# Kernel tuning notes

Hardware: AMD Instinct MI355X
Metric: run time of the kernel (lower is better)

## Reference

```python
import jax, jax.numpy as jnp
import numpy as np

B, C, T = 1024, 64, 512
D, H = 32, 4
DK = D // H  # 8
EPS = 1e-5


def setup_inputs() -> dict:
    key = jax.random.key(0)
    ks = jax.random.split(key, 10)
    s_in = 1.0 / np.sqrt(T)
    s_d = 1.0 / np.sqrt(D)
    return {
        "x": jax.random.normal(ks[0], (B, C, T), dtype=jnp.float32),
        "W_in": jax.random.uniform(ks[1], (T, D), jnp.float32, -s_in, s_in),
        "b_in": jax.random.uniform(ks[2], (D,), jnp.float32, -s_in, s_in),
        "W_q": jax.random.uniform(ks[3], (D, D), jnp.float32, -s_d, s_d),
        "W_k": jax.random.uniform(ks[4], (D, D), jnp.float32, -s_d, s_d),
        "W_v": jax.random.uniform(ks[5], (D, D), jnp.float32, -s_d, s_d),
        "W_out": jax.random.uniform(ks[6], (D, T), jnp.float32, -s_d, s_d),
        "b_out": jax.random.uniform(ks[7], (T,), jnp.float32, -s_d, s_d),
        "gamma": jnp.ones((T,), jnp.float32),
        "beta": jnp.zeros((T,), jnp.float32),
    }


def reference(x, W_in, b_in, W_q, W_k, W_v, W_out, b_out, gamma, beta):
    # x: (B, C, T) -> project time dim to d_model
    h = jnp.einsum("bct,td->bcd", x, W_in) + b_in  # (B,C,D)
    q = (h @ W_q).reshape(B, C, H, DK)
    k = (h @ W_k).reshape(B, C, H, DK)
    v = (h @ W_v).reshape(B, C, H, DK)
    # attention over channel axis; scores (B,H,C,C)
    scores = jnp.einsum("bchd,bkhd->bhck", q, k) / np.sqrt(DK).astype(np.float32)
    attn = jax.nn.softmax(scores, axis=-1)  # dropout is identity at inference
    out = jnp.einsum("bhck,bkhd->bchd", attn, v).reshape(B, C, D)
    out = out @ W_out + b_out  # (B,C,T); proj_out dropout is identity
    y = out + x  # residual
    mu = jnp.mean(y, axis=-1, keepdims=True)
    var = jnp.var(y, axis=-1, keepdims=True)
    return (y - mu) * jax.lax.rsqrt(var + EPS) * gamma + beta
```

## Files before the change

kernel.cpp:

```cpp
#include <hip/hip_runtime.h>

typedef __attribute__((ext_vector_type(8))) short bf16x8;
typedef __attribute__((ext_vector_type(4))) float f32x4;

#define NB 1024
#define NC 64
#define NT 512
#define ND 32
#define NH 4

__device__ __forceinline__ unsigned short f2bf(float f) {
  unsigned u = __float_as_uint(f);
  u += 0x7FFFu + ((u >> 16) & 1u);
  return (unsigned short)(u >> 16);
}

__global__ void prep_weights(const float* __restrict__ Win, const float* __restrict__ Wq,
                             const float* __restrict__ Wk, const float* __restrict__ Wv,
                             const float* __restrict__ Wout, unsigned short* __restrict__ ws) {
  int idx = blockIdx.x * 256 + threadIdx.x;
  if (idx >= 35840) return;
  float v;
  if (idx < 16384) {
    int j = idx & 7, lane = (idx >> 3) & 63, nt = (idx >> 9) & 1, ks = idx >> 10;
    int t = 32 * ks + 8 * (lane >> 4) + j;
    int d = 16 * nt + (lane & 15);
    v = Win[t * ND + d];
  } else if (idx < 32768) {
    int p = idx - 16384;
    int j = p & 7, lane = (p >> 3) & 63, nt = (p >> 9) & 31;
    int k = 8 * (lane >> 4) + j;
    int n = 16 * nt + (lane & 15);
    v = Wout[k * NT + n];
  } else {
    int p = idx - 32768;
    const float* W = (p < 1024) ? Wq : ((p < 2048) ? Wk : Wv);
    int q = p & 1023;
    int j = q & 7, lane = (q >> 3) & 63, nt = (q >> 9) & 1;
    int t = 8 * (lane >> 4) + j;
    int d = 16 * nt + (lane & 15);
    v = W[t * ND + d];
  }
  ws[idx] = f2bf(v);
}

__global__ __launch_bounds__(256, 2)
void mha_main(const float* __restrict__ x, const float* __restrict__ b_in,
              const float* __restrict__ b_out, const float* __restrict__ gamma,
              const float* __restrict__ beta, const unsigned short* __restrict__ wsb,
              float* __restrict__ out) {
  __shared__ __align__(16) unsigned short lds_h[4][64][8];
  __shared__ __align__(16) unsigned short lds_o[4][64][8];
  __shared__ __align__(16) float lds_q[64][36];
  __shared__ __align__(16) float lds_k[64][36];
  __shared__ __align__(16) float lds_v[64][36];
  __shared__ float lds_red0[4][64];
  __shared__ float lds_red1[4][64];
  __shared__ float lds_mu[64];
  __shared__ float lds_rs[64];

  const int tid = threadIdx.x;
  const int w  = tid >> 6;
  const int l  = tid & 63;
  const int g  = l >> 4;
  const int lo = l & 15;
  const int b  = blockIdx.x;
  const float* __restrict__ xb = x + (size_t)b * (NC * NT);

  const int srow = 16 * w + lo;
  const float* __restrict__ xr = xb + srow * NT + 8 * g;
  const bf16x8* __restrict__ wsWin = (const bf16x8*)wsb;

  f32x4 acc1[2];
  acc1[0] = (f32x4){0.f, 0.f, 0.f, 0.f};
  acc1[1] = (f32x4){0.f, 0.f, 0.f, 0.f};
  f32x4 ra = *(const f32x4*)(xr);
  f32x4 rb = *(const f32x4*)(xr + 4);
  bf16x8 bp0 = wsWin[l];
  bf16x8 bp1 = wsWin[64 + l];

#pragma unroll
  for (int ks = 0; ks < 16; ++ks) {
    bf16x8 af;
    af[0] = (short)f2bf(ra[0]); af[1] = (short)f2bf(ra[1]);
    af[2] = (short)f2bf(ra[2]); af[3] = (short)f2bf(ra[3]);
    af[4] = (short)f2bf(rb[0]); af[5] = (short)f2bf(rb[1]);
    af[6] = (short)f2bf(rb[2]); af[7] = (short)f2bf(rb[3]);
    int nk = (ks < 15) ? (ks + 1) : 15;
    f32x4 ra2 = *(const f32x4*)(xr + 32 * nk);
    f32x4 rb2 = *(const f32x4*)(xr + 32 * nk + 4);
    bf16x8 bn0 = wsWin[(2 * nk) * 64 + l];
    bf16x8 bn1 = wsWin[(2 * nk + 1) * 64 + l];
    acc1[0] = __builtin_amdgcn_mfma_f32_16x16x32_bf16(af, bp0, acc1[0], 0, 0, 0);
    acc1[1] = __builtin_amdgcn_mfma_f32_16x16x32_bf16(af, bp1, acc1[1], 0, 0, 0);
    ra = ra2; rb = rb2; bp0 = bn0; bp1 = bn1;
  }

  float binv0 = b_in[lo];
  float binv1 = b_in[16 + lo];
#pragma unroll
  for (int nt = 0; nt < 2; ++nt) {
#pragma unroll
    for (int r = 0; r < 4; ++r) {
      float hv = acc1[nt][r] + (nt ? binv1 : binv0);
      int cc = 2 * nt + (lo >> 3);
      int slotlane = (4 * g + r) | (cc << 4);
      lds_h[w][slotlane][lo & 7] = f2bf(hv);
    }
  }
  __syncthreads();

  const bf16x8* __restrict__ wsWq = (const bf16x8*)(wsb + 32768);
  const bf16x8* __restrict__ wsWk = (const bf16x8*)(wsb + 33792);
  const bf16x8* __restrict__ wsWv = (const bf16x8*)(wsb + 34816);
  bf16x8 ah = *(const bf16x8*)&lds_h[w][l][0];
  f32x4 zero4 = (f32x4){0.f, 0.f, 0.f, 0.f};
  f32x4 qacc[2], kacc[2], vacc[2];
#pragma unroll
  for (int nt = 0; nt < 2; ++nt) {
    qacc[nt] = __builtin_amdgcn_mfma_f32_16x16x32_bf16(ah, wsWq[nt * 64 + l], zero4, 0, 0, 0);
    kacc[nt] = __builtin_amdgcn_mfma_f32_16x16x32_bf16(ah, wsWk[nt * 64 + l], zero4, 0, 0, 0);
    vacc[nt] = __builtin_amdgcn_mfma_f32_16x16x32_bf16(ah, wsWv[nt * 64 + l], zero4, 0, 0, 0);
  }
#pragma unroll
  for (int nt = 0; nt < 2; ++nt) {
#pragma unroll
    for (int r = 0; r < 4; ++r) {
      int row = 16 * w + 4 * g + r;
      int col = 16 * nt + lo;
      lds_q[row][col] = qacc[nt][r];
      lds_k[row][col] = kacc[nt][r];
      lds_v[row][col] = vacc[nt][r];
    }
  }
  __syncthreads();

  {
    const int c = l, hd = w;
    const f32x4 qv0 = *(const f32x4*)&lds_q[c][8 * hd];
    const f32x4 qv1 = *(const f32x4*)&lds_q[c][8 * hd + 4];
    float sc[64];
    float mx = -3.4e38f;
#pragma unroll
    for (int kk = 0; kk < 64; ++kk) {
      f32x4 k0 = *(const f32x4*)&lds_k[kk][8 * hd];
      f32x4 k1 = *(const f32x4*)&lds_k[kk][8 * hd + 4];
      float s = qv0[0] * k0[0] + qv0[1] * k0[1] + qv0[2] * k0[2] + qv0[3] * k0[3]
              + qv1[0] * k1[0] + qv1[1] * k1[1] + qv1[2] * k1[2] + qv1[3] * k1[3];
      s *= 0.35355339059327373f;
      sc[kk] = s;
      mx = fmaxf(mx, s);
    }
    float sum = 0.f;
#pragma unroll
    for (int kk = 0; kk < 64; ++kk) {
      float p = exp2f((sc[kk] - mx) * 1.4426950408889634f);
      sc[kk] = p;
      sum += p;
    }
    float inv = 1.0f / sum;
    float ov[8] = {0.f, 0.f, 0.f, 0.f, 0.f, 0.f, 0.f, 0.f};
#pragma unroll
    for (int kk = 0; kk < 64; ++kk) {
      f32x4 v0 = *(const f32x4*)&lds_v[kk][8 * hd];
      f32x4 v1 = *(const f32x4*)&lds_v[kk][8 * hd + 4];
      float p = sc[kk];
      ov[0] += p * v0[0]; ov[1] += p * v0[1]; ov[2] += p * v0[2]; ov[3] += p * v0[3];
      ov[4] += p * v1[0]; ov[5] += p * v1[1]; ov[6] += p * v1[2]; ov[7] += p * v1[3];
    }
    bf16x8 opk;
#pragma unroll
    for (int d = 0; d < 8; ++d) opk[d] = (short)f2bf(ov[d] * inv);
    *(bf16x8*)&lds_o[c >> 4][(c & 15) | (hd << 4)][0] = opk;
  }
  __syncthreads();

  bf16x8 a4[4];
#pragma unroll
  for (int mt = 0; mt < 4; ++mt) a4[mt] = *(const bf16x8*)&lds_o[mt][l][0];
  const bf16x8* __restrict__ wsWout = (const bf16x8*)(wsb + 16384);
  f32x4 acc[4][8];
#pragma unroll
  for (int mt = 0; mt < 4; ++mt)
#pragma unroll
    for (int nt = 0; nt < 8; ++nt) acc[mt][nt] = zero4;
#pragma unroll
  for (int nt = 0; nt < 8; ++nt) {
    bf16x8 bfr = wsWout[(8 * w + nt) * 64 + l];
#pragma unroll
    for (int mt = 0; mt < 4; ++mt)
      acc[mt][nt] = __builtin_amdgcn_mfma_f32_16x16x32_bf16(a4[mt], bfr, acc[mt][nt], 0, 0, 0);
  }

  const int colbase = 128 * w + lo;
  float bo[8], gm[8], bt[8];
#pragma unroll
  for (int nt = 0; nt < 8; ++nt) {
    int col = colbase + 16 * nt;
    bo[nt] = b_out[col];
    gm[nt] = gamma[col];
    bt[nt] = beta[col];
  }

  float s1[4][4], s2[4][4];
#pragma unroll
  for (int mt = 0; mt < 4; ++mt)
#pragma unroll
    for (int r = 0; r < 4; ++r) { s1[mt][r] = 0.f; s2[mt][r] = 0.f; }

#pragma unroll
  for (int mt = 0; mt < 4; ++mt) {
#pragma unroll
    for (int r = 0; r < 4; ++r) {
      int row = 16 * mt + 4 * g + r;
      const float* __restrict__ xrow = xb + row * NT + colbase;
#pragma unroll
      for (int nt = 0; nt < 8; ++nt) {
        float y = acc[mt][nt][r] + bo[nt] + xrow[16 * nt];
        acc[mt][nt][r] = y;
        s1[mt][r] += y;
        s2[mt][r] += y * y;
      }
    }
  }
#pragma unroll
  for (int off = 1; off <= 8; off <<= 1) {
#pragma unroll
    for (int mt = 0; mt < 4; ++mt)
#pragma unroll
      for (int r = 0; r < 4; ++r) {
        s1[mt][r] += __shfl_xor(s1[mt][r], off, 64);
        s2[mt][r] += __shfl_xor(s2[mt][r], off, 64);
      }
  }
#pragma unroll
  for (int mt = 0; mt < 4; ++mt)
#pragma unroll
    for (int r = 0; r < 4; ++r)
      if (lo == (r * 4 + mt)) {
        int row = 16 * mt + 4 * g + r;
        lds_red0[w][row] = s1[mt][r];
        lds_red1[w][row] = s2[mt][r];
      }
  __syncthreads();
  if (tid < 64) {
    float s = lds_red0[0][tid] + lds_red0[1][tid] + lds_red0[2][tid] + lds_red0[3][tid];
    float q2 = lds_red1[0][tid] + lds_red1[1][tid] + lds_red1[2][tid] + lds_red1[3][tid];
    float mu = s * (1.0f / 512.0f);
    float var = q2 * (1.0f / 512.0f) - mu * mu;
    lds_mu[tid] = mu;
    lds_rs[tid] = rsqrtf(var + 1e-5f);
  }
  __syncthreads();

  float* __restrict__ ob = out + (size_t)b * (NC * NT);
#pragma unroll
  for (int mt = 0; mt < 4; ++mt) {
#pragma unroll
    for (int r = 0; r < 4; ++r) {
      int row = 16 * mt + 4 * g + r;
      float mu = lds_mu[row], rs = lds_rs[row];
      float* __restrict__ orow = ob + row * NT + colbase;
#pragma unroll
      for (int nt = 0; nt < 8; ++nt)
        orow[16 * nt] = (acc[mt][nt][r] - mu) * rs * gm[nt] + bt[nt];
    }
  }
}

extern "C" void kernel_launch(void* const* d_in, const int* in_sizes, int n_in,
                              void* d_out, int out_size, void* d_ws, size_t ws_size,
                              hipStream_t stream) {
  const float* x     = (const float*)d_in[0];
  const float* W_in  = (const float*)d_in[1];
  const float* b_in  = (const float*)d_in[2];
  const float* W_q   = (const float*)d_in[3];
  const float* W_k   = (const float*)d_in[4];
  const float* W_v   = (const float*)d_in[5];
  const float* W_out = (const float*)d_in[6];
  const float* b_out = (const float*)d_in[7];
  const float* gamma = (const float*)d_in[8];
  const float* beta  = (const float*)d_in[9];
  unsigned short* ws = (unsigned short*)d_ws;

  prep_weights<<<140, 256, 0, stream>>>(W_in, W_q, W_k, W_v, W_out, ws);
  mha_main<<<NB, 256, 0, stream>>>(x, b_in, b_out, gamma, beta, ws, (float*)d_out);
}
```

Baseline: 88.39 us.

## Stage x tile in LDS as swizzled bf16 and reuse it for the residual

New measurement: 151.4 us. 71.3% more time.

```diff
diff --git a/kernel.cpp b/kernel.cpp
--- a/kernel.cpp
+++ b/kernel.cpp
@@ -7,12 +7,14 @@
 #define NC 64
 #define NT 512
 #define ND 32
-#define NH 4
 
 __device__ __forceinline__ unsigned short f2bf(float f) {
   unsigned u = __float_as_uint(f);
   u += 0x7FFFu + ((u >> 16) & 1u);
   return (unsigned short)(u >> 16);
+}
+__device__ __forceinline__ float bf2f(unsigned short h) {
+  return __uint_as_float(((unsigned)h) << 16);
 }
 
 __global__ void prep_weights(const float* __restrict__ Win, const float* __restrict__ Wq,
@@ -49,15 +51,9 @@
               const float* __restrict__ b_out, const float* __restrict__ gamma,
               const float* __restrict__ beta, const unsigned short* __restrict__ wsb,
               float* __restrict__ out) {
-  __shared__ __align__(16) unsigned short lds_h[4][64][8];
-  __shared__ __align__(16) unsigned short lds_o[4][64][8];
-  __shared__ __align__(16) float lds_q[64][36];
-  __shared__ __align__(16) float lds_k[64][36];
-  __shared__ __align__(16) float lds_v[64][36];
-  __shared__ float lds_red0[4][64];
-  __shared__ float lds_red1[4][64];
-  __shared__ float lds_mu[64];
-  __shared__ float lds_rs[64];
+  __shared__ __align__(16) unsigned short x_lds[32768];
+  __shared__ __align__(16) unsigned short ho_lds[4][64][8];
+  __shared__ __align__(16) unsigned short qkv_lds[6144];
 
   const int tid = threadIdx.x;
   const int w  = tid >> 6;
@@ -67,33 +63,39 @@
   const int b  = blockIdx.x;
   const float* __restrict__ xb = x + (size_t)b * (NC * NT);
 
+  char* const xbase = (char*)x_lds;
+
+#pragma unroll
+  for (int it = 0; it < 16; ++it) {
+    int id = it * 256 + tid;
+    int row = id >> 6;
+    int c = id & 63;
+    const float* src = xb + row * NT + c * 8;
+    f32x4 A = *(const f32x4*)src;
+    f32x4 Bv = *(const f32x4*)(src + 4);
+    bf16x8 pk;
+    pk[0] = (short)f2bf(A[0]);  pk[1] = (short)f2bf(A[1]);
+    pk[2] = (short)f2bf(A[2]);  pk[3] = (short)f2bf(A[3]);
+    pk[4] = (short)f2bf(Bv[0]); pk[5] = (short)f2bf(Bv[1]);
+    pk[6] = (short)f2bf(Bv[2]); pk[7] = (short)f2bf(Bv[3]);
+    *(bf16x8*)(xbase + ((row << 10) | ((c << 4) ^ ((row & 7) << 4)))) = pk;
+  }
+  __syncthreads();
+
   const int srow = 16 * w + lo;
-  const float* __restrict__ xr = xb + srow * NT + 8 * g;
+  const int arow_base = srow << 10;
+  const int aswz = (srow & 7) << 4;
   const bf16x8* __restrict__ wsWin = (const bf16x8*)wsb;
 
+  f32x4 zero4 = (f32x4){0.f, 0.f, 0.f, 0.f};
   f32x4 acc1[2];
-  acc1[0] = (f32x4){0.f, 0.f, 0.f, 0.f};
-  acc1[1] = (f32x4){0.f, 0.f, 0.f, 0.f};
-  f32x4 ra = *(const f32x4*)(xr);
-  f32x4 rb = *(const f32x4*)(xr + 4);
-  bf16x8 bp0 = wsWin[l];
-  bf16x8 bp1 = wsWin[64 + l];
-
+  acc1[0] = zero4;
+  acc1[1] = zero4;
 #pragma unroll
   for (int ks = 0; ks < 16; ++ks) {
-    bf16x8 af;
-    af[0] = (short)f2bf(ra[0]); af[1] = (short)f2bf(ra[1]);
-    af[2] = (short)f2bf(ra[2]); af[3] = (short)f2bf(ra[3]);
-    af[4] = (short)f2bf(rb[0]); af[5] = (short)f2bf(rb[1]);
-    af[6] = (short)f2bf(rb[2]); af[7] = (short)f2bf(rb[3]);
-    int nk = (ks < 15) ? (ks + 1) : 15;
-    f32x4 ra2 = *(const f32x4*)(xr + 32 * nk);
-    f32x4 rb2 = *(const f32x4*)(xr + 32 * nk + 4);
-    bf16x8 bn0 = wsWin[(2 * nk) * 64 + l];
-    bf16x8 bn1 = wsWin[(2 * nk + 1) * 64 + l];
-    acc1[0] = __builtin_amdgcn_mfma_f32_16x16x32_bf16(af, bp0, acc1[0], 0, 0, 0);
-    acc1[1] = __builtin_amdgcn_mfma_f32_16x16x32_bf16(af, bp1, acc1[1], 0, 0, 0);
-    ra = ra2; rb = rb2; bp0 = bn0; bp1 = bn1;
+    bf16x8 af = *(const bf16x8*)(xbase + (arow_base | (((ks << 6) | (g << 4)) ^ aswz)));
+    acc1[0] = __builtin_amdgcn_mfma_f32_16x16x32_bf16(af, wsWin[(2 * ks) * 64 + l], acc1[0], 0, 0, 0);
+    acc1[1] = __builtin_amdgcn_mfma_f32_16x16x32_bf16(af, wsWin[(2 * ks + 1) * 64 + l], acc1[1], 0, 0, 0);
   }
 
   float binv0 = b_in[lo];
@@ -105,7 +107,7 @@
       float hv = acc1[nt][r] + (nt ? binv1 : binv0);
       int cc = 2 * nt + (lo >> 3);
       int slotlane = (4 * g + r) | (cc << 4);
-      lds_h[w][slotlane][lo & 7] = f2bf(hv);
+      ho_lds[w][slotlane][lo & 7] = f2bf(hv);
     }
   }
   __syncthreads();
@@ -113,8 +115,7 @@
   const bf16x8* __restrict__ wsWq = (const bf16x8*)(wsb + 32768);
   const bf16x8* __restrict__ wsWk = (const bf16x8*)(wsb + 33792);
   const bf16x8* __restrict__ wsWv = (const bf16x8*)(wsb + 34816);
-  bf16x8 ah = *(const bf16x8*)&lds_h[w][l][0];
-  f32x4 zero4 = (f32x4){0.f, 0.f, 0.f, 0.f};
+  bf16x8 ah = *(const bf16x8*)&ho_lds[w][l][0];
   f32x4 qacc[2], kacc[2], vacc[2];
 #pragma unroll
   for (int nt = 0; nt < 2; ++nt) {
@@ -122,31 +123,36 @@
     kacc[nt] = __builtin_amdgcn_mfma_f32_16x16x32_bf16(ah, wsWk[nt * 64 + l], zero4, 0, 0, 0);
     vacc[nt] = __builtin_amdgcn_mfma_f32_16x16x32_bf16(ah, wsWv[nt * 64 + l], zero4, 0, 0, 0);
   }
+  unsigned short* q_l = qkv_lds;
+  unsigned short* k_l = qkv_lds + 2048;
+  unsigned short* v_l = qkv_lds + 4096;
 #pragma unroll
   for (int nt = 0; nt < 2; ++nt) {
 #pragma unroll
     for (int r = 0; r < 4; ++r) {
       int row = 16 * w + 4 * g + r;
       int col = 16 * nt + lo;
-      lds_q[row][col] = qacc[nt][r];
-      lds_k[row][col] = kacc[nt][r];
-      lds_v[row][col] = vacc[nt][r];
+      q_l[row * 32 + col] = f2bf(qacc[nt][r]);
+      k_l[row * 32 + col] = f2bf(kacc[nt][r]);
+      v_l[row * 32 + col] = f2bf(vacc[nt][r]);
     }
   }
   __syncthreads();
 
   {
     const int c = l, hd = w;
-    const f32x4 qv0 = *(const f32x4*)&lds_q[c][8 * hd];
-    const f32x4 qv1 = *(const f32x4*)&lds_q[c][8 * hd + 4];
+    bf16x8 q8 = *(const bf16x8*)&q_l[c * 32 + 8 * hd];
+    float qv[8];
+#pragma unroll
+    for (int d = 0; d < 8; ++d) qv[d] = bf2f((unsigned short)q8[d]);
     float sc[64];
     float mx = -3.4e38f;
 #pragma unroll
     for (int kk = 0; kk < 64; ++kk) {
-      f32x4 k0 = *(const f32x4*)&lds_k[kk][8 * hd];
-      f32x4 k1 = *(const f32x4*)&lds_k[kk][8 * hd + 4];
-      float s = qv0[0] * k0[0] + qv0[1] * k0[1] + qv0[2] * k0[2] + qv0[3] * k0[3]
-              + qv1[0] * k1[0] + qv1[1] * k1[1] + qv1[2] * k1[2] + qv1[3] * k1[3];
+      bf16x8 k8 = *(const bf16x8*)&k_l[kk * 32 + 8 * hd];
+      float s = 0.f;
+#pragma unroll
+      for (int d = 0; d < 8; ++d) s += qv[d] * bf2f((unsigned short)k8[d]);
       s *= 0.35355339059327373f;
       sc[kk] = s;
       mx = fmaxf(mx, s);
@@ -162,22 +168,21 @@
     float ov[8] = {0.f, 0.f, 0.f, 0.f, 0.f, 0.f, 0.f, 0.f};
 #pragma unroll
     for (int kk = 0; kk < 64; ++kk) {
-      f32x4 v0 = *(const f32x4*)&lds_v[kk][8 * hd];
-      f32x4 v1 = *(const f32x4*)&lds_v[kk][8 * hd + 4];
+      bf16x8 v8 = *(const bf16x8*)&v_l[kk * 32 + 8 * hd];
       float p = sc[kk];
-      ov[0] += p * v0[0]; ov[1] += p * v0[1]; ov[2] += p * v0[2]; ov[3] += p * v0[3];
-      ov[4] += p * v1[0]; ov[5] += p * v1[1]; ov[6] += p * v1[2]; ov[7] += p * v1[3];
+#pragma unroll
+      for (int d = 0; d < 8; ++d) ov[d] += p * bf2f((unsigned short)v8[d]);
     }
     bf16x8 opk;
 #pragma unroll
     for (int d = 0; d < 8; ++d) opk[d] = (short)f2bf(ov[d] * inv);
-    *(bf16x8*)&lds_o[c >> 4][(c & 15) | (hd << 4)][0] = opk;
+    *(bf16x8*)&ho_lds[c >> 4][(c & 15) | (hd << 4)][0] = opk;
   }
   __syncthreads();
 
   bf16x8 a4[4];
 #pragma unroll
-  for (int mt = 0; mt < 4; ++mt) a4[mt] = *(const bf16x8*)&lds_o[mt][l][0];
+  for (int mt = 0; mt < 4; ++mt) a4[mt] = *(const bf16x8*)&ho_lds[mt][l][0];
   const bf16x8* __restrict__ wsWout = (const bf16x8*)(wsb + 16384);
   f32x4 acc[4][8];
 #pragma unroll
@@ -213,10 +218,13 @@
 #pragma unroll
     for (int r = 0; r < 4; ++r) {
       int row = 16 * mt + 4 * g + r;
-      const float* __restrict__ xrow = xb + row * NT + colbase;
+      int rbase = row << 10;
+      int rsz = (row & 7) << 4;
 #pragma unroll
       for (int nt = 0; nt < 8; ++nt) {
-        float y = acc[mt][nt][r] + bo[nt] + xrow[16 * nt];
+        int colb = 2 * (colbase + 16 * nt);
+        unsigned short xr16 = *(const unsigned short*)(xbase + (rbase | (colb ^ rsz)));
+        float y = acc[mt][nt][r] + bo[nt] + bf2f(xr16);
         acc[mt][nt][r] = y;
         s1[mt][r] += y;
         s2[mt][r] += y * y;
@@ -233,23 +241,27 @@
         s2[mt][r] += __shfl_xor(s2[mt][r], off, 64);
       }
   }
+  float* red0 = (float*)qkv_lds;
+  float* red1 = red0 + 256;
+  float* mu_a = red0 + 512;
+  float* rs_a = red0 + 576;
 #pragma unroll
   for (int mt = 0; mt < 4; ++mt)
 #pragma unroll
     for (int r = 0; r < 4; ++r)
       if (lo == (r * 4 + mt)) {
         int row = 16 * mt + 4 * g + r;
-        lds_red0[w][row] = s1[mt][r];
-        lds_red1[w][row] = s2[mt][r];
+        red0[w * 64 + row] = s1[mt][r];
+        red1[w * 64 + row] = s2[mt][r];
       }
   __syncthreads();
   if (tid < 64) {
-    float s = lds_red0[0][tid] + lds_red0[1][tid] + lds_red0[2][tid] + lds_red0[3][tid];
-    float q2 = lds_red1[0][tid] + lds_red1[1][tid] + lds_red1[2][tid] + lds_red1[3][tid];
+    float s = red0[tid] + red0[64 + tid] + red0[128 + tid] + red0[192 + tid];
+    float q2 = red1[tid] + red1[64 + tid] + red1[128 + tid] + red1[192 + tid];
     float mu = s * (1.0f / 512.0f);
     float var = q2 * (1.0f / 512.0f) - mu * mu;
-    lds_mu[tid] = mu;
-    lds_rs[tid] = rsqrtf(var + 1e-5f);
+    mu_a[tid] = mu;
+    rs_a[tid] = rsqrtf(var + 1e-5f);
   }
   __syncthreads();
 
@@ -259,7 +271,7 @@
 #pragma unroll
     for (int r = 0; r < 4; ++r) {
       int row = 16 * mt + 4 * g + r;
-      float mu = lds_mu[row], rs = lds_rs[row];
+      float mu = mu_a[row], rs = rs_a[row];
       float* __restrict__ orow = ob + row * NT + colbase;
 #pragma unroll
       for (int nt = 0; nt < 8; ++nt)
```

## Split fused attention kernel into two kernels staging output in output buffer

Applied to the files above, without the earlier changes.

New measurement: 94.34 us. +6.7%, slower.

```diff
diff --git a/kernel.cpp b/kernel.cpp
--- a/kernel.cpp
+++ b/kernel.cpp
@@ -7,7 +7,6 @@
 #define NC 64
 #define NT 512
 #define ND 32
-#define NH 4
 
 __device__ __forceinline__ unsigned short f2bf(float f) {
   unsigned u = __float_as_uint(f);
@@ -44,20 +43,13 @@
   ws[idx] = f2bf(v);
 }
 
-__global__ __launch_bounds__(256, 2)
-void mha_main(const float* __restrict__ x, const float* __restrict__ b_in,
-              const float* __restrict__ b_out, const float* __restrict__ gamma,
-              const float* __restrict__ beta, const unsigned short* __restrict__ wsb,
-              float* __restrict__ out) {
+__global__ __launch_bounds__(256, 4)
+void mha_a(const float* __restrict__ x, const float* __restrict__ b_in,
+           const unsigned short* __restrict__ wsb, float* __restrict__ ostash) {
   __shared__ __align__(16) unsigned short lds_h[4][64][8];
-  __shared__ __align__(16) unsigned short lds_o[4][64][8];
   __shared__ __align__(16) float lds_q[64][36];
   __shared__ __align__(16) float lds_k[64][36];
   __shared__ __align__(16) float lds_v[64][36];
-  __shared__ float lds_red0[4][64];
-  __shared__ float lds_red1[4][64];
-  __shared__ float lds_mu[64];
-  __shared__ float lds_rs[64];
 
   const int tid = threadIdx.x;
   const int w  = tid >> 6;
@@ -71,9 +63,10 @@
   const float* __restrict__ xr = xb + srow * NT + 8 * g;
   const bf16x8* __restrict__ wsWin = (const bf16x8*)wsb;
 
+  f32x4 zero4 = (f32x4){0.f, 0.f, 0.f, 0.f};
   f32x4 acc1[2];
-  acc1[0] = (f32x4){0.f, 0.f, 0.f, 0.f};
-  acc1[1] = (f32x4){0.f, 0.f, 0.f, 0.f};
+  acc1[0] = zero4;
+  acc1[1] = zero4;
   f32x4 ra = *(const f32x4*)(xr);
   f32x4 rb = *(const f32x4*)(xr + 4);
   bf16x8 bp0 = wsWin[l];
@@ -114,7 +107,6 @@
   const bf16x8* __restrict__ wsWk = (const bf16x8*)(wsb + 33792);
   const bf16x8* __restrict__ wsWv = (const bf16x8*)(wsb + 34816);
   bf16x8 ah = *(const bf16x8*)&lds_h[w][l][0];
-  f32x4 zero4 = (f32x4){0.f, 0.f, 0.f, 0.f};
   f32x4 qacc[2], kacc[2], vacc[2];
 #pragma unroll
   for (int nt = 0; nt < 2; ++nt) {
@@ -171,14 +163,37 @@
     bf16x8 opk;
 #pragma unroll
     for (int d = 0; d < 8; ++d) opk[d] = (short)f2bf(ov[d] * inv);
-    *(bf16x8*)&lds_o[c >> 4][(c & 15) | (hd << 4)][0] = opk;
-  }
-  __syncthreads();
-
+    unsigned short* __restrict__ osb =
+        (unsigned short*)(ostash + (size_t)b * (NC * NT)) + 63488;
+    *(bf16x8*)(osb + ((c >> 4) * 64 + ((c & 15) | (hd << 4))) * 8) = opk;
+  }
+}
+
+__global__ __launch_bounds__(256, 2)
+void mha_b(const float* __restrict__ x, const float* __restrict__ b_out,
+           const float* __restrict__ gamma, const float* __restrict__ beta,
+           const unsigned short* __restrict__ wsb, float* __restrict__ out) {
+  __shared__ float red0[4][64];
+  __shared__ float red1[4][64];
+  __shared__ float mu_a[64];
+  __shared__ float rs_a[64];
+
+  const int tid = threadIdx.x;
+  const int w  = tid >> 6;
+  const int l  = tid & 63;
+  const int g  = l >> 4;
+  const int lo = l & 15;
+  const int b  = blockIdx.x;
+  const float* __restrict__ xb = x + (size_t)b * (NC * NT);
+  float* __restrict__ ob = out + (size_t)b * (NC * NT);
+
+  const unsigned short* __restrict__ osb = (const unsigned short*)ob + 63488;
   bf16x8 a4[4];
 #pragma unroll
-  for (int mt = 0; mt < 4; ++mt) a4[mt] = *(const bf16x8*)&lds_o[mt][l][0];
+  for (int mt = 0; mt < 4; ++mt) a4[mt] = *(const bf16x8*)(osb + (mt * 64 + l) * 8);
+
   const bf16x8* __restrict__ wsWout = (const bf16x8*)(wsb + 16384);
+  f32x4 zero4 = (f32x4){0.f, 0.f, 0.f, 0.f};
   f32x4 acc[4][8];
 #pragma unroll
   for (int mt = 0; mt < 4; ++mt)
@@ -239,27 +254,26 @@
     for (int r = 0; r < 4; ++r)
       if (lo == (r * 4 + mt)) {
         int row = 16 * mt + 4 * g + r;
-        lds_red0[w][row] = s1[mt][r];
-        lds_red1[w][row] = s2[mt][r];
+        red0[w][row] = s1[mt][r];
+        red1[w][row] = s2[mt][r];
       }
   __syncthreads();
   if (tid < 64) {
-    float s = lds_red0[0][tid] + lds_red0[1][tid] + lds_red0[2][tid] + lds_red0[3][tid];
-    float q2 = lds_red1[0][tid] + lds_red1[1][tid] + lds_red1[2][tid] + lds_red1[3][tid];
+    float s = red0[0][tid] + red0[1][tid] + red0[2][tid] + red0[3][tid];
+    float q2 = red1[0][tid] + red1[1][tid] + red1[2][tid] + red1[3][tid];
     float mu = s * (1.0f / 512.0f);
     float var = q2 * (1.0f / 512.0f) - mu * mu;
-    lds_mu[tid] = mu;
-    lds_rs[tid] = rsqrtf(var + 1e-5f);
+    mu_a[tid] = mu;
+    rs_a[tid] = rsqrtf(var + 1e-5f);
   }
   __syncthreads();
 
-  float* __restrict__ ob = out + (size_t)b * (NC * NT);
 #pragma unroll
   for (int mt = 0; mt < 4; ++mt) {
 #pragma unroll
     for (int r = 0; r < 4; ++r) {
       int row = 16 * mt + 4 * g + r;
-      float mu = lds_mu[row], rs = lds_rs[row];
+      float mu = mu_a[row], rs = rs_a[row];
       float* __restrict__ orow = ob + row * NT + colbase;
 #pragma unroll
       for (int nt = 0; nt < 8; ++nt)
@@ -284,5 +298,6 @@
   unsigned short* ws = (unsigned short*)d_ws;
 
   prep_weights<<<140, 256, 0, stream>>>(W_in, W_q, W_k, W_v, W_out, ws);
-  mha_main<<<NB, 256, 0, stream>>>(x, b_in, b_out, gamma, beta, ws, (float*)d_out);
-}
+  mha_a<<<NB, 256, 0, stream>>>(x, b_in, ws, (float*)d_out);
+  mha_b<<<NB, 256, 0, stream>>>(x, b_out, gamma, beta, ws, (float*)d_out);
+}
```

## Recompute output projection in second pass to cut registers and raise occupancy

Applied to the files above, without the earlier changes.

New measurement: 306.8 us. 3.47x slower.

```diff
diff --git a/kernel.cpp b/kernel.cpp
--- a/kernel.cpp
+++ b/kernel.cpp
@@ -7,7 +7,6 @@
 #define NC 64
 #define NT 512
 #define ND 32
-#define NH 4
 
 __device__ __forceinline__ unsigned short f2bf(float f) {
   unsigned u = __float_as_uint(f);
@@ -44,20 +43,15 @@
   ws[idx] = f2bf(v);
 }
 
-__global__ __launch_bounds__(256, 2)
+__global__ __launch_bounds__(256, 4)
 void mha_main(const float* __restrict__ x, const float* __restrict__ b_in,
               const float* __restrict__ b_out, const float* __restrict__ gamma,
               const float* __restrict__ beta, const unsigned short* __restrict__ wsb,
               float* __restrict__ out) {
-  __shared__ __align__(16) unsigned short lds_h[4][64][8];
-  __shared__ __align__(16) unsigned short lds_o[4][64][8];
+  __shared__ __align__(16) unsigned short lds_ho[4][64][8];
   __shared__ __align__(16) float lds_q[64][36];
   __shared__ __align__(16) float lds_k[64][36];
   __shared__ __align__(16) float lds_v[64][36];
-  __shared__ float lds_red0[4][64];
-  __shared__ float lds_red1[4][64];
-  __shared__ float lds_mu[64];
-  __shared__ float lds_rs[64];
 
   const int tid = threadIdx.x;
   const int w  = tid >> 6;
@@ -71,9 +65,10 @@
   const float* __restrict__ xr = xb + srow * NT + 8 * g;
   const bf16x8* __restrict__ wsWin = (const bf16x8*)wsb;
 
+  f32x4 zero4 = (f32x4){0.f, 0.f, 0.f, 0.f};
   f32x4 acc1[2];
-  acc1[0] = (f32x4){0.f, 0.f, 0.f, 0.f};
-  acc1[1] = (f32x4){0.f, 0.f, 0.f, 0.f};
+  acc1[0] = zero4;
+  acc1[1] = zero4;
   f32x4 ra = *(const f32x4*)(xr);
   f32x4 rb = *(const f32x4*)(xr + 4);
   bf16x8 bp0 = wsWin[l];
@@ -105,7 +100,7 @@
       float hv = acc1[nt][r] + (nt ? binv1 : binv0);
       int cc = 2 * nt + (lo >> 3);
       int slotlane = (4 * g + r) | (cc << 4);
-      lds_h[w][slotlane][lo & 7] = f2bf(hv);
+      lds_ho[w][slotlane][lo & 7] = f2bf(hv);
     }
   }
   __syncthreads();
@@ -113,8 +108,7 @@
   const bf16x8* __restrict__ wsWq = (const bf16x8*)(wsb + 32768);
   const bf16x8* __restrict__ wsWk = (const bf16x8*)(wsb + 33792);
   const bf16x8* __restrict__ wsWv = (const bf16x8*)(wsb + 34816);
-  bf16x8 ah = *(const bf16x8*)&lds_h[w][l][0];
-  f32x4 zero4 = (f32x4){0.f, 0.f, 0.f, 0.f};
+  bf16x8 ah = *(const bf16x8*)&lds_ho[w][l][0];
   f32x4 qacc[2], kacc[2], vacc[2];
 #pragma unroll
   for (int nt = 0; nt < 2; ++nt) {
@@ -171,53 +165,44 @@
     bf16x8 opk;
 #pragma unroll
     for (int d = 0; d < 8; ++d) opk[d] = (short)f2bf(ov[d] * inv);
-    *(bf16x8*)&lds_o[c >> 4][(c & 15) | (hd << 4)][0] = opk;
-  }
-  __syncthreads();
+    *(bf16x8*)&lds_ho[c >> 4][(c & 15) | (hd << 4)][0] = opk;
+  }
+  __syncthreads();
+
+  float* red0 = &lds_q[0][0];
+  float* red1 = red0 + 256;
+  float* mu_a = red0 + 512;
+  float* rs_a = red0 + 576;
 
   bf16x8 a4[4];
 #pragma unroll
-  for (int mt = 0; mt < 4; ++mt) a4[mt] = *(const bf16x8*)&lds_o[mt][l][0];
+  for (int mt = 0; mt < 4; ++mt) a4[mt] = *(const bf16x8*)&lds_ho[mt][l][0];
   const bf16x8* __restrict__ wsWout = (const bf16x8*)(wsb + 16384);
-  f32x4 acc[4][8];
+
+  const int colbase = 128 * w + lo;
+  float bo[8];
+#pragma unroll
+  for (int nt = 0; nt < 8; ++nt) bo[nt] = b_out[colbase + 16 * nt];
+
+  float s1[4][4], s2[4][4];
 #pragma unroll
   for (int mt = 0; mt < 4; ++mt)
 #pragma unroll
-    for (int nt = 0; nt < 8; ++nt) acc[mt][nt] = zero4;
+    for (int r = 0; r < 4; ++r) { s1[mt][r] = 0.f; s2[mt][r] = 0.f; }
+
 #pragma unroll
   for (int nt = 0; nt < 8; ++nt) {
     bf16x8 bfr = wsWout[(8 * w + nt) * 64 + l];
+    f32x4 acc[4];
 #pragma unroll
     for (int mt = 0; mt < 4; ++mt)
-      acc[mt][nt] = __builtin_amdgcn_mfma_f32_16x16x32_bf16(a4[mt], bfr, acc[mt][nt], 0, 0, 0);
-  }
-
-  const int colbase = 128 * w + lo;
-  float bo[8], gm[8], bt[8];
-#pragma unroll
-  for (int nt = 0; nt < 8; ++nt) {
-    int col = colbase + 16 * nt;
-    bo[nt] = b_out[col];
-    gm[nt] = gamma[col];
-    bt[nt] = beta[col];
-  }
-
-  float s1[4][4], s2[4][4];
-#pragma unroll
-  for (int mt = 0; mt < 4; ++mt)
-#pragma unroll
-    for (int r = 0; r < 4; ++r) { s1[mt][r] = 0.f; s2[mt][r] = 0.f; }
-
-#pragma unroll
-  for (int mt = 0; mt < 4; ++mt) {
-#pragma unroll
-    for (int r = 0; r < 4; ++r) {
-      int row = 16 * mt + 4 * g + r;
-      const float* __restrict__ xrow = xb + row * NT + colbase;
-#pragma unroll
-      for (int nt = 0; nt < 8; ++nt) {
-        float y = acc[mt][nt][r] + bo[nt] + xrow[16 * nt];
-        acc[mt][nt][r] = y;
+      acc[mt] = __builtin_amdgcn_mfma_f32_16x16x32_bf16(a4[mt], bfr, zero4, 0, 0, 0);
+#pragma unroll
+    for (int mt = 0; mt < 4; ++mt) {
+#pragma unroll
+      for (int r = 0; r < 4; ++r) {
+        int row = 16 * mt + 4 * g + r;
+        float y = acc[mt][r] + bo[nt] + xb[row * NT + colbase + 16 * nt];
         s1[mt][r] += y;
         s2[mt][r] += y * y;
       }
@@ -239,31 +224,42 @@
     for (int r = 0; r < 4; ++r)
       if (lo == (r * 4 + mt)) {
         int row = 16 * mt + 4 * g + r;
-        lds_red0[w][row] = s1[mt][r];
-        lds_red1[w][row] = s2[mt][r];
+        red0[w * 64 + row] = s1[mt][r];
+        red1[w * 64 + row] = s2[mt][r];
       }
   __syncthreads();
   if (tid < 64) {
-    float s = lds_red0[0][tid] + lds_red0[1][tid] + lds_red0[2][tid] + lds_red0[3][tid];
-    float q2 = lds_red1[0][tid] + lds_red1[1][tid] + lds_red1[2][tid] + lds_red1[3][tid];
+    float s = red0[tid] + red0[64 + tid] + red0[128 + tid] + red0[192 + tid];
+    float q2 = red1[tid] + red1[64 + tid] + red1[128 + tid] + red1[192 + tid];
     float mu = s * (1.0f / 512.0f);
     float var = q2 * (1.0f / 512.0f) - mu * mu;
-    lds_mu[tid] = mu;
-    lds_rs[tid] = rsqrtf(var + 1e-5f);
-  }
-  __syncthreads();
-
+    mu_a[tid] = mu;
+    rs_a[tid] = rsqrtf(var + 1e-5f);
+  }
+  __syncthreads();
+
+  float gm[8], bt[8];
+#pragma unroll
+  for (int nt = 0; nt < 8; ++nt) {
+    gm[nt] = gamma[colbase + 16 * nt];
+    bt[nt] = beta[colbase + 16 * nt];
+  }
   float* __restrict__ ob = out + (size_t)b * (NC * NT);
 #pragma unroll
-  for (int mt = 0; mt < 4; ++mt) {
-#pragma unroll
-    for (int r = 0; r < 4; ++r) {
-      int row = 16 * mt + 4 * g + r;
-      float mu = lds_mu[row], rs = lds_rs[row];
-      float* __restrict__ orow = ob + row * NT + colbase;
-#pragma unroll
-      for (int nt = 0; nt < 8; ++nt)
-        orow[16 * nt] = (acc[mt][nt][r] - mu) * rs * gm[nt] + bt[nt];
+  for (int nt = 0; nt < 8; ++nt) {
+    bf16x8 bfr = wsWout[(8 * w + nt) * 64 + l];
+    f32x4 acc[4];
+#pragma unroll
+    for (int mt = 0; mt < 4; ++mt)
+      acc[mt] = __builtin_amdgcn_mfma_f32_16x16x32_bf16(a4[mt], bfr, zero4, 0, 0, 0);
+#pragma unroll
+    for (int mt = 0; mt < 4; ++mt) {
+#pragma unroll
+      for (int r = 0; r < 4; ++r) {
+        int row = 16 * mt + 4 * g + r;
+        float y = acc[mt][r] + bo[nt] + xb[row * NT + colbase + 16 * nt];
+        ob[row * NT + colbase + 16 * nt] = (y - mu_a[row]) * rs_a[row] * gm[nt] + bt[nt];
+      }
     }
   }
 }
```
